# Kernel tuning notes

Hardware: AMD Instinct MI355X
Metric: run time of the kernel (lower is better)

## Reference

```python
import jax, jax.numpy as jnp
import numpy as np

NUM_HEADS = 16

def setup_inputs() -> dict:
    key = jax.random.key(0)
    ks = jax.random.split(key, 11)
    S, B, E = 2048, 2, 1024
    scale = 1.0 / np.sqrt(E)
    return {
        "query": jax.random.normal(ks[0], (S, B, E), dtype=jnp.float32),
        "key":   jax.random.normal(ks[1], (S, B, E), dtype=jnp.float32),
        "value": jax.random.normal(ks[2], (S, B, E), dtype=jnp.float32),
        "Wq": jax.random.normal(ks[3], (E, E), dtype=jnp.float32) * scale,
        "bq": jax.random.normal(ks[4], (E,), dtype=jnp.float32) * 0.02,
        "Wk": jax.random.normal(ks[5], (E, E), dtype=jnp.float32) * scale,
        "bk": jax.random.normal(ks[6], (E,), dtype=jnp.float32) * 0.02,
        "Wv": jax.random.normal(ks[7], (E, E), dtype=jnp.float32) * scale,
        "bv": jax.random.normal(ks[8], (E,), dtype=jnp.float32) * 0.02,
        "Wo": jax.random.normal(ks[9], (E, E), dtype=jnp.float32) * scale,
        "bo": jax.random.normal(ks[10], (E,), dtype=jnp.float32) * 0.02,
    }

def _batch_invariant_softmax(x):
    # max-shift, exp in input dtype, sum/divide in float32, cast back
    x_max = jnp.max(x, axis=-1, keepdims=True)
    exp_x = jnp.exp(x - x_max).astype(jnp.float32)
    return (exp_x / jnp.sum(exp_x, axis=-1, keepdims=True)).astype(x.dtype)

def reference(query, key, value, Wq, bq, Wk, bk, Wv, bv, Wo, bo):
    S, B, E = query.shape
    H = NUM_HEADS
    D = E // H
    scale = 1.0 / np.sqrt(D)
    # projections (torch Linear: y = x @ W.T + b)
    q = query @ Wq.T + bq   # [S,B,E]
    k = key   @ Wk.T + bk
    v = value @ Wv.T + bv
    # [S,B,E] -> [B,H,S,D]
    q = q.reshape(S, B, H, D).transpose(1, 2, 0, 3)
    k = k.reshape(-1, B, H, D).transpose(1, 2, 0, 3)
    v = v.reshape(-1, B, H, D).transpose(1, 2, 0, 3)
    scores = jnp.einsum('bhqd,bhkd->bhqk', q, k) * scale  # [B,H,S,S]
    causal = jnp.triu(jnp.ones((S, S), dtype=bool), k=1)
    scores = jnp.where(causal, -jnp.inf, scores)
    attn = _batch_invariant_softmax(scores)
    out = jnp.einsum('bhqk,bhkd->bhqd', attn, v)  # [B,H,S,D]
    out = out.transpose(2, 0, 1, 3).reshape(S, B, E)  # [S,B,E]
    return out @ Wo.T + bo
```

## Files before the change

kernel.cpp:

```cpp
#include <hip/hip_runtime.h>
#include <cstddef>
#include <cstdint>

#define S_LEN 2048
#define B_SZ  2
#define E_SZ  1024
#define H_NUM 16
#define D_HEAD 64
#define M_ROWS 4096
#define NEG_BIG (-1e30f)

typedef __attribute__((ext_vector_type(8))) short bf16x8;
typedef __attribute__((ext_vector_type(4))) float f32x4;

#define P_QRYH (0ull << 20)
#define P_QRYL (8ull << 20)
#define P_KEYH (16ull << 20)
#define P_KEYL (24ull << 20)
#define P_VALH (32ull << 20)
#define P_VALL (40ull << 20)
#define P_WQH  (48ull << 20)
#define P_WQL  (50ull << 20)
#define P_WKH  (52ull << 20)
#define P_WKL  (54ull << 20)
#define P_WVH  (56ull << 20)
#define P_WVL  (58ull << 20)
#define P_WOH  (60ull << 20)
#define P_WOL  (62ull << 20)
#define P_QPH  (64ull << 20)
#define P_QPL  (72ull << 20)
#define P_KPH  (80ull << 20)
#define P_KPL  (88ull << 20)
#define P_VTH  (96ull << 20)
#define P_VTL  (104ull << 20)
#define P_AOH  (0ull << 20)
#define P_AOL  (8ull << 20)

__device__ __forceinline__ unsigned short rtne_bf16(float f) {
    unsigned int u = __float_as_uint(f);
    return (unsigned short)((u + 0x7fffu + ((u >> 16) & 1u)) >> 16);
}

__device__ __forceinline__ void split1(float f, unsigned short &h, unsigned short &l) {
    const unsigned int u = __float_as_uint(f);
    h = (unsigned short)(u >> 16);
    l = rtne_bf16(f - __uint_as_float(u & 0xffff0000u));
}

__device__ __forceinline__ void split4(const float4 v, ushort4 &h, ushort4 &l) {
    const unsigned int ux = __float_as_uint(v.x);
    const unsigned int uy = __float_as_uint(v.y);
    const unsigned int uz = __float_as_uint(v.z);
    const unsigned int uw = __float_as_uint(v.w);
    h.x = (unsigned short)(ux >> 16);
    h.y = (unsigned short)(uy >> 16);
    h.z = (unsigned short)(uz >> 16);
    h.w = (unsigned short)(uw >> 16);
    l.x = rtne_bf16(v.x - __uint_as_float(ux & 0xffff0000u));
    l.y = rtne_bf16(v.y - __uint_as_float(uy & 0xffff0000u));
    l.z = rtne_bf16(v.z - __uint_as_float(uz & 0xffff0000u));
    l.w = rtne_bf16(v.w - __uint_as_float(uw & 0xffff0000u));
}

__device__ __forceinline__ void gl16(const void* g, void* l) {
    __builtin_amdgcn_global_load_lds(
        (const __attribute__((address_space(1))) void*)g,
        (__attribute__((address_space(3))) void*)l, 16, 0, 0);
}

__global__ __launch_bounds__(256) void split_planes(
    const float* __restrict__ q, const float* __restrict__ k, const float* __restrict__ v,
    const float* __restrict__ wq, const float* __restrict__ wk,
    const float* __restrict__ wv, const float* __restrict__ wo,
    unsigned char* __restrict__ ws)
{
    const int z = blockIdx.y;
    const float* src; size_t oh, ol; int n;
    switch (z) {
        case 0: src = q;  oh = P_QRYH; ol = P_QRYL; n = 4194304; break;
        case 1: src = k;  oh = P_KEYH; ol = P_KEYL; n = 4194304; break;
        case 2: src = v;  oh = P_VALH; ol = P_VALL; n = 4194304; break;
        case 3: src = wq; oh = P_WQH;  ol = P_WQL;  n = 1048576; break;
        case 4: src = wk; oh = P_WKH;  ol = P_WKL;  n = 1048576; break;
        case 5: src = wv; oh = P_WVH;  ol = P_WVL;  n = 1048576; break;
        default:src = wo; oh = P_WOH;  ol = P_WOL;  n = 1048576; break;
    }
    const int i = blockIdx.x * 256 + threadIdx.x;
    if (i * 4 >= n) return;
    float4 vv = *(const float4*)&src[(size_t)i * 4];
    ushort4 h, l;
    split4(vv, h, l);
    *(ushort4*)(ws + oh + (size_t)i * 8) = h;
    *(ushort4*)(ws + ol + (size_t)i * 8) = l;
}

__global__ __launch_bounds__(256, 3) void gemm_qkv_planes(
    const float* __restrict__ bq, const float* __restrict__ bk, const float* __restrict__ bv,
    unsigned char* __restrict__ ws)
{
    __shared__ unsigned short AH[4096], AL[4096], WH[4096], WL[4096];

    const int z = blockIdx.z;
    const unsigned char* aph = ws + (z == 0 ? P_QRYH : z == 1 ? P_KEYH : P_VALH);
    const unsigned char* apl = ws + (z == 0 ? P_QRYL : z == 1 ? P_KEYL : P_VALL);
    const unsigned char* wph = ws + (z == 0 ? P_WQH : z == 1 ? P_WKH : P_WVH);
    const unsigned char* wpl = ws + (z == 0 ? P_WQL : z == 1 ? P_WKL : P_WVL);
    const float* bias = z == 0 ? bq : z == 1 ? bk : bv;

    const int t = threadIdx.x, lid = t & 63, w = t >> 6;
    const int wr = w >> 1, wc = w & 1, g = lid >> 4, r16 = lid & 15;
    const int m0 = blockIdx.x * 128, n0 = blockIdx.y * 128;

    const int lrow = lid >> 2;
    const int cA = (lid & 3) ^ (lrow & 3);

    int offA[4], offW[4];
#pragma unroll
    for (int m = 0; m < 4; ++m)
        offA[m] = (wr * 64 + m * 16 + r16) * 32 + ((g ^ (r16 & 3)) << 3);
#pragma unroll
    for (int n = 0; n < 4; ++n)
        offW[n] = (wc * 64 + n * 16 + r16) * 32 + ((g ^ (r16 & 3)) << 3);

    f32x4 acc[4][4];
    const f32x4 zero = {0.f, 0.f, 0.f, 0.f};
#pragma unroll
    for (int m = 0; m < 4; ++m)
#pragma unroll
        for (int n = 0; n < 4; ++n) acc[m][n] = zero;

    for (int kt = 0; kt < 1024; kt += 32) {
        __syncthreads();
#pragma unroll
        for (int i = 0; i < 2; ++i) {
            const int ra = m0 + w * 32 + i * 16 + lrow;
            const size_t ab = (size_t)ra * 2048 + (size_t)kt * 2 + (size_t)cA * 16;
            gl16(aph + ab, &AH[(w * 32 + i * 16) * 32]);
            gl16(apl + ab, &AL[(w * 32 + i * 16) * 32]);
            const int rw = n0 + w * 32 + i * 16 + lrow;
            const size_t wb = (size_t)rw * 2048 + (size_t)kt * 2 + (size_t)cA * 16;
            gl16(wph + wb, &WH[(w * 32 + i * 16) * 32]);
            gl16(wpl + wb, &WL[(w * 32 + i * 16) * 32]);
        }
        __syncthreads();

        bf16x8 ah[4], al[4], whf[4], wlf[4];
#pragma unroll
        for (int m = 0; m < 4; ++m) {
            ah[m] = *(const bf16x8*)&AH[offA[m]];
            al[m] = *(const bf16x8*)&AL[offA[m]];
        }
#pragma unroll
        for (int n = 0; n < 4; ++n) {
            whf[n] = *(const bf16x8*)&WH[offW[n]];
            wlf[n] = *(const bf16x8*)&WL[offW[n]];
        }
#pragma unroll
        for (int m = 0; m < 4; ++m)
#pragma unroll
            for (int n = 0; n < 4; ++n) {
                acc[m][n] = __builtin_amdgcn_mfma_f32_16x16x32_bf16(ah[m], whf[n], acc[m][n], 0, 0, 0);
                acc[m][n] = __builtin_amdgcn_mfma_f32_16x16x32_bf16(ah[m], wlf[n], acc[m][n], 0, 0, 0);
                acc[m][n] = __builtin_amdgcn_mfma_f32_16x16x32_bf16(al[m], whf[n], acc[m][n], 0, 0, 0);
            }
    }

    float bn[4];
#pragma unroll
    for (int n = 0; n < 4; ++n) bn[n] = bias[n0 + wc * 64 + n * 16 + r16];

    if (z < 2) {
        unsigned short* ph = (unsigned short*)(ws + (z == 0 ? P_QPH : P_KPH));
        unsigned short* pl = (unsigned short*)(ws + (z == 0 ? P_QPL : P_KPL));
#pragma unroll
        for (int m = 0; m < 4; ++m)
#pragma unroll
            for (int n = 0; n < 4; ++n) {
                const int col = n0 + wc * 64 + n * 16 + r16;
                const int hh = col >> 6, d = col & 63;
#pragma unroll
                for (int r = 0; r < 4; ++r) {
                    const int tok = m0 + wr * 64 + m * 16 + g * 4 + r;
                    const int s = tok >> 1, b = tok & 1;
                    unsigned short vh, vl;
                    split1(acc[m][n][r] + bn[n], vh, vl);
                    const size_t idx = ((size_t)((b * 16 + hh) * 2048 + s)) * 64 + d;
                    ph[idx] = vh; pl[idx] = vl;
                }
            }
    } else {
        unsigned short* ph = (unsigned short*)(ws + P_VTH);
        unsigned short* pl = (unsigned short*)(ws + P_VTL);
#pragma unroll
        for (int m = 0; m < 4; ++m)
#pragma unroll
            for (int n = 0; n < 4; ++n) {
                const int col = n0 + wc * 64 + n * 16 + r16;
                const int hh = col >> 6, d = col & 63;
                const int tok0 = m0 + wr * 64 + m * 16 + g * 4;
                const int s0 = tok0 >> 1;
                unsigned short vh[4], vl[4];
#pragma unroll
                for (int r = 0; r < 4; ++r) split1(acc[m][n][r] + bn[n], vh[r], vl[r]);
                const size_t i0 = ((size_t)((0  + hh) * 64 + d)) * 2048 + s0;
                const size_t i1 = ((size_t)((16 + hh) * 64 + d)) * 2048 + s0;
                ushort2 u;
                u.x = vh[0]; u.y = vh[2]; *(ushort2*)&ph[i0] = u;
                u.x = vh[1]; u.y = vh[3]; *(ushort2*)&ph[i1] = u;
                u.x = vl[0]; u.y = vl[2]; *(ushort2*)&pl[i0] = u;
                u.x = vl[1]; u.y = vl[3]; *(ushort2*)&pl[i1] = u;
            }
    }
}

__global__ __launch_bounds__(256, 2) void gemm_out_planes(
    const float* __restrict__ bo, const unsigned char* __restrict__ ws,
    float* __restrict__ out)
{
    __shared__ unsigned short AH[2048], AL[2048], WH[4096], WL[4096];

    const unsigned char* aph = ws + P_AOH;
    const unsigned char* apl = ws + P_AOL;
    const unsigned char* wph = ws + P_WOH;
    const unsigned char* wpl = ws + P_WOL;

    const int t = threadIdx.x, lid = t & 63, w = t >> 6;
    const int wr = w >> 1, wc = w & 1, g = lid >> 4, r16 = lid & 15;
    const int m0 = blockIdx.x * 64, n0 = blockIdx.y * 128;
    const int lrow = lid >> 2;
    const int cA = (lid & 3) ^ (lrow & 3);

    int offA[2], offW[4];
#pragma unroll
    for (int m = 0; m < 2; ++m)
        offA[m] = (wr * 32 + m * 16 + r16) * 32 + ((g ^ (r16 & 3)) << 3);
#pragma unroll
    for (int n = 0; n < 4; ++n)
        offW[n] = (wc * 64 + n * 16 + r16) * 32 + ((g ^ (r16 & 3)) << 3);

    f32x4 acc[2][4];
    const f32x4 zero = {0.f, 0.f, 0.f, 0.f};
#pragma unroll
    for (int m = 0; m < 2; ++m)
#pragma unroll
        for (int n = 0; n < 4; ++n) acc[m][n] = zero;

    for (int kt = 0; kt < 1024; kt += 32) {
        __syncthreads();
        {
            const int ra = m0 + w * 16 + lrow;
            const size_t ab = (size_t)ra * 2048 + (size_t)kt * 2 + (size_t)cA * 16;
            gl16(aph + ab, &AH[(w * 16) * 32]);
            gl16(apl + ab, &AL[(w * 16) * 32]);
        }
#pragma unroll
        for (int i = 0; i < 2; ++i) {
            const int rw = n0 + w * 32 + i * 16 + lrow;
            const size_t wb = (size_t)rw * 2048 + (size_t)kt * 2 + (size_t)cA * 16;
            gl16(wph + wb, &WH[(w * 32 + i * 16) * 32]);
            gl16(wpl + wb, &WL[(w * 32 + i * 16) * 32]);
        }
        __syncthreads();

        bf16x8 ah[2], al[2], whf[4], wlf[4];
#pragma unroll
        for (int m = 0; m < 2; ++m) {
            ah[m] = *(const bf16x8*)&AH[offA[m]];
            al[m] = *(const bf16x8*)&AL[offA[m]];
        }
#pragma unroll
        for (int n = 0; n < 4; ++n) {
            whf[n] = *(const bf16x8*)&WH[offW[n]];
            wlf[n] = *(const bf16x8*)&WL[offW[n]];
        }
#pragma unroll
        for (int m = 0; m < 2; ++m)
#pragma unroll
            for (int n = 0; n < 4; ++n) {
                acc[m][n] = __builtin_amdgcn_mfma_f32_16x16x32_bf16(ah[m], whf[n], acc[m][n], 0, 0, 0);
                acc[m][n] = __builtin_amdgcn_mfma_f32_16x16x32_bf16(ah[m], wlf[n], acc[m][n], 0, 0, 0);
                acc[m][n] = __builtin_amdgcn_mfma_f32_16x16x32_bf16(al[m], whf[n], acc[m][n], 0, 0, 0);
            }
    }

    float bn[4];
#pragma unroll
    for (int n = 0; n < 4; ++n) bn[n] = bo[n0 + wc * 64 + n * 16 + r16];
#pragma unroll
    for (int m = 0; m < 2; ++m)
#pragma unroll
        for (int n = 0; n < 4; ++n) {
            const int col = n0 + wc * 64 + n * 16 + r16;
#pragma unroll
            for (int r = 0; r < 4; ++r) {
                const int row = m0 + wr * 32 + m * 16 + g * 4 + r;
                out[(size_t)row * 1024 + col] = acc[m][n][r] + bn[n];
            }
        }
}

__global__ __launch_bounds__(256, 2) void attn_fwd(unsigned char* __restrict__ ws)
{
    __shared__ unsigned short sm[40960];

    const int t = threadIdx.x, lid = t & 63, w = t >> 6;
    const int g = lid >> 4, r16 = lid & 15;
    const int bh = blockIdx.y;
    const int b = bh >> 4, h = bh & 15;

    const unsigned char* qhp  = ws + P_QPH + (size_t)bh * 262144;
    const unsigned char* qlp  = ws + P_QPL + (size_t)bh * 262144;
    const unsigned char* khp  = ws + P_KPH + (size_t)bh * 262144;
    const unsigned char* klp  = ws + P_KPL + (size_t)bh * 262144;
    const unsigned char* vthp = ws + P_VTH + (size_t)bh * 262144;
    const unsigned char* vtlp = ws + P_VTL + (size_t)bh * 262144;
    unsigned short* aoh = (unsigned short*)(ws + P_AOH);
    unsigned short* aol = (unsigned short*)(ws + P_AOL);

    const int lrow = lid >> 3;
    const int cK = (lid & 7) ^ lrow;
    const float scale = 0.125f;

    int offF[4][2], offQ[2], offP[4][4];
#pragma unroll
    for (int nf = 0; nf < 4; ++nf)
#pragma unroll
        for (int ks = 0; ks < 2; ++ks)
            offF[nf][ks] = (nf * 16 + r16) * 64 + (((ks * 4 + g) ^ (r16 & 7)) << 3);
#pragma unroll
    for (int ks = 0; ks < 2; ++ks)
        offQ[ks] = (w * 16 + r16) * 64 + (((ks * 4 + g) ^ (r16 & 7)) << 3);
#pragma unroll
    for (int nf = 0; nf < 4; ++nf)
#pragma unroll
        for (int r = 0; r < 4; ++r) {
            const int rp = w * 16 + g * 4 + r;
            offP[nf][r] = rp * 64 + (((nf * 2 + (r16 >> 3)) ^ (rp & 7)) << 3) + (r16 & 7);
        }

    auto stage_kv = [&](int bsel, int tt) {
#pragma unroll
        for (int i = 0; i < 2; ++i) {
            const int r = w * 16 + i * 8 + lrow;
            const int db = bsel * 16384 + (w * 16 + i * 8) * 64;
            const size_t kb = (size_t)(tt * 64 + r) * 128 + (size_t)cK * 16;
            gl16(khp + kb, &sm[db]);
            gl16(klp + kb, &sm[db + 4096]);
            const size_t vb = (size_t)r * 4096 + (size_t)tt * 128 + (size_t)cK * 16;
            gl16(vthp + vb, &sm[db + 8192]);
            gl16(vtlp + vb, &sm[db + 12288]);
        }
    };

    const f32x4 zero = {0.f, 0.f, 0.f, 0.f};

    for (int pass = 0; pass < 2; ++pass) {
        const int qt = (pass == 0) ? blockIdx.x : 31 - blockIdx.x;
        const int q0 = qt * 64;

#pragma unroll
        for (int i = 0; i < 2; ++i) {
            const int r = w * 16 + i * 8 + lrow;
            const size_t qb = (size_t)(q0 + r) * 128 + (size_t)cK * 16;
            gl16(qhp + qb, &sm[32768 + (w * 16 + i * 8) * 64]);
            gl16(qlp + qb, &sm[36864 + (w * 16 + i * 8) * 64]);
        }
        stage_kv(0, 0);
        __syncthreads();

        bf16x8 qh[2], ql[2];
#pragma unroll
        for (int ks = 0; ks < 2; ++ks) {
            qh[ks] = *(const bf16x8*)&sm[32768 + offQ[ks]];
            ql[ks] = *(const bf16x8*)&sm[36864 + offQ[ks]];
        }

        f32x4 oacc[4];
        float m_r[4], l_r[4];
#pragma unroll
        for (int i = 0; i < 4; ++i) { oacc[i] = zero; m_r[i] = NEG_BIG; l_r[i] = 0.f; }

        for (int tt = 0; tt <= qt; ++tt) {
            const int bb = (tt & 1) * 16384;
            const int k0 = tt * 64;
            if (tt < qt) stage_kv((tt & 1) ^ 1, tt + 1);

            f32x4 sacc[4];
#pragma unroll
            for (int nf = 0; nf < 4; ++nf) sacc[nf] = zero;
#pragma unroll
            for (int nf = 0; nf < 4; ++nf)
#pragma unroll
                for (int ks = 0; ks < 2; ++ks) {
                    bf16x8 kh = *(const bf16x8*)&sm[bb + offF[nf][ks]];
                    bf16x8 kl = *(const bf16x8*)&sm[bb + 4096 + offF[nf][ks]];
                    sacc[nf] = __builtin_amdgcn_mfma_f32_16x16x32_bf16(qh[ks], kh, sacc[nf], 0, 0, 0);
                    sacc[nf] = __builtin_amdgcn_mfma_f32_16x16x32_bf16(qh[ks], kl, sacc[nf], 0, 0, 0);
                    sacc[nf] = __builtin_amdgcn_mfma_f32_16x16x32_bf16(ql[ks], kh, sacc[nf], 0, 0, 0);
                }

            float rm[4] = {NEG_BIG, NEG_BIG, NEG_BIG, NEG_BIG};
#pragma unroll
            for (int nf = 0; nf < 4; ++nf) {
                const int k_abs = k0 + nf * 16 + r16;
#pragma unroll
                for (int r = 0; r < 4; ++r) {
                    const int q_abs = q0 + w * 16 + g * 4 + r;
                    float val = sacc[nf][r] * scale;
                    if (k_abs > q_abs) val = NEG_BIG;
                    sacc[nf][r] = val;
                    rm[r] = fmaxf(rm[r], val);
                }
            }
#pragma unroll
            for (int off = 1; off < 16; off <<= 1)
#pragma unroll
                for (int r = 0; r < 4; ++r)
                    rm[r] = fmaxf(rm[r], __shfl_xor(rm[r], off, 64));

            float scf[4];
#pragma unroll
            for (int r = 0; r < 4; ++r) {
                const float mn = fmaxf(m_r[r], rm[r]);
                scf[r] = __expf(m_r[r] - mn);
                m_r[r] = mn;
            }

            float pv4[4][4];
            float rs[4] = {0.f, 0.f, 0.f, 0.f};
#pragma unroll
            for (int nf = 0; nf < 4; ++nf)
#pragma unroll
                for (int r = 0; r < 4; ++r) {
                    const float p = __expf(sacc[nf][r] - m_r[r]);
                    pv4[nf][r] = p;
                    rs[r] += p;
                }
#pragma unroll
            for (int off = 1; off < 16; off <<= 1)
#pragma unroll
                for (int r = 0; r < 4; ++r)
                    rs[r] += __shfl_xor(rs[r], off, 64);

#pragma unroll
            for (int r = 0; r < 4; ++r) {
                l_r[r] = l_r[r] * scf[r] + rs[r];
#pragma unroll
                for (int nf = 0; nf < 4; ++nf) oacc[nf][r] *= scf[r];
            }

#pragma unroll
            for (int nf = 0; nf < 4; ++nf)
#pragma unroll
                for (int r = 0; r < 4; ++r) {
                    unsigned short h1, l1;
                    split1(pv4[nf][r], h1, l1);
                    sm[32768 + offP[nf][r]] = h1;
                    sm[36864 + offP[nf][r]] = l1;
                }

#pragma unroll
            for (int ks = 0; ks < 2; ++ks) {
                bf16x8 pah = *(const bf16x8*)&sm[32768 + offQ[ks]];
                bf16x8 pal = *(const bf16x8*)&sm[36864 + offQ[ks]];
#pragma unroll
                for (int nf = 0; nf < 4; ++nf) {
                    bf16x8 vh = *(const bf16x8*)&sm[bb + 8192 + offF[nf][ks]];
                    bf16x8 vl = *(const bf16x8*)&sm[bb + 12288 + offF[nf][ks]];
                    oacc[nf] = __builtin_amdgcn_mfma_f32_16x16x32_bf16(pah, vh, oacc[nf], 0, 0, 0);
                    oacc[nf] = __builtin_amdgcn_mfma_f32_16x16x32_bf16(pah, vl, oacc[nf], 0, 0, 0);
                    oacc[nf] = __builtin_amdgcn_mfma_f32_16x16x32_bf16(pal, vh, oacc[nf], 0, 0, 0);
                }
            }
            __syncthreads();
        }

        float inv[4];
#pragma unroll
        for (int r = 0; r < 4; ++r) inv[r] = 1.0f / l_r[r];
#pragma unroll
        for (int nf = 0; nf < 4; ++nf) {
            const int d = nf * 16 + r16;
#pragma unroll
            for (int r = 0; r < 4; ++r) {
                const int s = q0 + w * 16 + g * 4 + r;
                unsigned short hh, ll;
                split1(oacc[nf][r] * inv[r], hh, ll);
                const size_t idx = (size_t)(s * 2 + b) * 1024 + h * 64 + d;
                aoh[idx] = hh; aol[idx] = ll;
            }
        }
    }
}

extern "C" void kernel_launch(void* const* d_in, const int* in_sizes, int n_in,
                              void* d_out, int out_size, void* d_ws, size_t ws_size,
                              hipStream_t stream)
{
    const float* query = (const float*)d_in[0];
    const float* key   = (const float*)d_in[1];
    const float* value = (const float*)d_in[2];
    const float* Wq = (const float*)d_in[3];  const float* bq = (const float*)d_in[4];
    const float* Wk = (const float*)d_in[5];  const float* bk = (const float*)d_in[6];
    const float* Wv = (const float*)d_in[7];  const float* bv = (const float*)d_in[8];
    const float* Wo = (const float*)d_in[9];  const float* bo = (const float*)d_in[10];
    float* out = (float*)d_out;
    unsigned char* ws = (unsigned char*)d_ws;
    (void)ws_size; (void)in_sizes; (void)n_in; (void)out_size;

    const dim3 tb(256);

    split_planes<<<dim3(4096, 7), tb, 0, stream>>>(query, key, value, Wq, Wk, Wv, Wo, ws);
    gemm_qkv_planes<<<dim3(32, 8, 3), tb, 0, stream>>>(bq, bk, bv, ws);
    attn_fwd<<<dim3(16, 32), tb, 0, stream>>>(ws);
    gemm_out_planes<<<dim3(64, 8), tb, 0, stream>>>(bo, ws, out);
}
```

Before: 344.2 us.

## Fold softmax scale into Q projection, mask only diagonal tile, remap attention grid

Folds the 1/sqrt(D) scale into the Q projection epilogue, which removes the per-score multiply in attention. The causal mask is now applied only on the diagonal tile, and the row max is computed directly from the accumulators. The attention launch becomes a 1D grid of 512 blocks with a swizzled mapping that interleaves heads across blocks, likely for XCD/L2 locality. s_setprio hints are added around the MFMA sections to favor matrix issue. Pre-scaling Q by 0.125, an exact power of two, before the hi/lo bf16 split keeps the precision the same.

Measured after the change: 351.5 us. 1.02x slower.

```diff
diff --git a/kernel.cpp b/kernel.cpp
--- a/kernel.cpp
+++ b/kernel.cpp
@@ -106,6 +106,7 @@
     const unsigned char* wph = ws + (z == 0 ? P_WQH : z == 1 ? P_WKH : P_WVH);
     const unsigned char* wpl = ws + (z == 0 ? P_WQL : z == 1 ? P_WKL : P_WVL);
     const float* bias = z == 0 ? bq : z == 1 ? bk : bv;
+    const float postscale = (z == 0) ? 0.125f : 1.0f;
 
     const int t = threadIdx.x, lid = t & 63, w = t >> 6;
     const int wr = w >> 1, wc = w & 1, g = lid >> 4, r16 = lid & 15;
@@ -183,7 +184,7 @@
                     const int tok = m0 + wr * 64 + m * 16 + g * 4 + r;
                     const int s = tok >> 1, b = tok & 1;
                     unsigned short vh, vl;
-                    split1(acc[m][n][r] + bn[n], vh, vl);
+                    split1((acc[m][n][r] + bn[n]) * postscale, vh, vl);
                     const size_t idx = ((size_t)((b * 16 + hh) * 2048 + s)) * 64 + d;
                     ph[idx] = vh; pl[idx] = vl;
                 }
@@ -305,7 +306,11 @@
 
     const int t = threadIdx.x, lid = t & 63, w = t >> 6;
     const int g = lid >> 4, r16 = lid & 15;
-    const int bh = blockIdx.y;
+
+    const int c = blockIdx.x;
+    const int logical = (c & 7) * 64 + (c >> 3);
+    const int bh = logical >> 4;
+    const int xq = logical & 15;
     const int b = bh >> 4, h = bh & 15;
 
     const unsigned char* qhp  = ws + P_QPH + (size_t)bh * 262144;
@@ -319,7 +324,6 @@
 
     const int lrow = lid >> 3;
     const int cK = (lid & 7) ^ lrow;
-    const float scale = 0.125f;
 
     int offF[4][2], offQ[2], offP[4][4];
 #pragma unroll
@@ -355,7 +359,7 @@
     const f32x4 zero = {0.f, 0.f, 0.f, 0.f};
 
     for (int pass = 0; pass < 2; ++pass) {
-        const int qt = (pass == 0) ? blockIdx.x : 31 - blockIdx.x;
+        const int qt = (pass == 0) ? xq : 31 - xq;
         const int q0 = qt * 64;
 
 #pragma unroll
@@ -382,12 +386,12 @@
 
         for (int tt = 0; tt <= qt; ++tt) {
             const int bb = (tt & 1) * 16384;
-            const int k0 = tt * 64;
             if (tt < qt) stage_kv((tt & 1) ^ 1, tt + 1);
 
             f32x4 sacc[4];
 #pragma unroll
             for (int nf = 0; nf < 4; ++nf) sacc[nf] = zero;
+            __builtin_amdgcn_s_setprio(1);
 #pragma unroll
             for (int nf = 0; nf < 4; ++nf)
 #pragma unroll
@@ -398,20 +402,24 @@
                     sacc[nf] = __builtin_amdgcn_mfma_f32_16x16x32_bf16(qh[ks], kl, sacc[nf], 0, 0, 0);
                     sacc[nf] = __builtin_amdgcn_mfma_f32_16x16x32_bf16(ql[ks], kh, sacc[nf], 0, 0, 0);
                 }
-
-            float rm[4] = {NEG_BIG, NEG_BIG, NEG_BIG, NEG_BIG};
-#pragma unroll
-            for (int nf = 0; nf < 4; ++nf) {
-                const int k_abs = k0 + nf * 16 + r16;
-#pragma unroll
-                for (int r = 0; r < 4; ++r) {
-                    const int q_abs = q0 + w * 16 + g * 4 + r;
-                    float val = sacc[nf][r] * scale;
-                    if (k_abs > q_abs) val = NEG_BIG;
-                    sacc[nf][r] = val;
-                    rm[r] = fmaxf(rm[r], val);
+            __builtin_amdgcn_s_setprio(0);
+
+            if (tt == qt) {
+#pragma unroll
+                for (int nf = 0; nf < 4; ++nf) {
+                    const int k_loc = nf * 16 + r16;
+#pragma unroll
+                    for (int r = 0; r < 4; ++r) {
+                        const int q_loc = w * 16 + g * 4 + r;
+                        if (k_loc > q_loc) sacc[nf][r] = NEG_BIG;
+                    }
                 }
             }
+
+            float rm[4];
+#pragma unroll
+            for (int r = 0; r < 4; ++r)
+                rm[r] = fmaxf(fmaxf(sacc[0][r], sacc[1][r]), fmaxf(sacc[2][r], sacc[3][r]));
 #pragma unroll
             for (int off = 1; off < 16; off <<= 1)
 #pragma unroll
@@ -459,6 +467,7 @@
                     sm[36864 + offP[nf][r]] = l1;
                 }
 
+            __builtin_amdgcn_s_setprio(1);
 #pragma unroll
             for (int ks = 0; ks < 2; ++ks) {
                 bf16x8 pah = *(const bf16x8*)&sm[32768 + offQ[ks]];
@@ -472,6 +481,7 @@
                     oacc[nf] = __builtin_amdgcn_mfma_f32_16x16x32_bf16(pal, vh, oacc[nf], 0, 0, 0);
                 }
             }
+            __builtin_amdgcn_s_setprio(0);
             __syncthreads();
         }
 
@@ -512,6 +522,6 @@
 
     split_planes<<<dim3(4096, 7), tb, 0, stream>>>(query, key, value, Wq, Wk, Wv, Wo, ws);
     gemm_qkv_planes<<<dim3(32, 8, 3), tb, 0, stream>>>(bq, bk, bv, ws);
-    attn_fwd<<<dim3(16, 32), tb, 0, stream>>>(ws);
+    attn_fwd<<<dim3(512), tb, 0, stream>>>(ws);
     gemm_out_planes<<<dim3(64, 8), tb, 0, stream>>>(bo, ws, out);
 }
```
